# Optimization experiments

Hardware: AMD Instinct MI355X
Metric: run time of the kernel (lower is better)

## Reference

```python
import math
import jax, jax.numpy as jnp
import numpy as np

# Module hyperparameters (match init_kwargs)
EMBED = 512
H = 8            # n_heads
D = EMBED // H   # head_dim = 64
P = 32           # poly_dim
M = 4            # num_prf_features
R = 1            # num_quadrature_nodes
B = 1
T = 1024
EPS = 1e-6
C_CONST = 2.0 + EPS
# Gauss-Laguerre nodes/weights (R=1 -> node=1, weight=1), scaled by 1/C as in __init__
_nodes_np, _weights_np = np.polynomial.laguerre.laggauss(R)
QUAD_NODES = (_nodes_np / C_CONST).astype(np.float32)   # [R]


def setup_inputs() -> dict:
    key = jax.random.key(0)
    ks = jax.random.split(key, 6)
    x = jax.random.normal(ks[0], (B, T, EMBED), dtype=jnp.float32)
    qkv_w = jax.random.normal(ks[1], (3 * EMBED, EMBED), dtype=jnp.float32) * 0.02
    qkv_b = jnp.zeros((3 * EMBED,), dtype=jnp.float32)
    out_w = jax.random.normal(ks[2], (EMBED, EMBED), dtype=jnp.float32) * 0.02
    out_b = jnp.zeros((EMBED,), dtype=jnp.float32)
    omega = jax.random.normal(ks[3], (R, H, D, M), dtype=jnp.float32)  # PRF projection buffer
    poly_proj = jax.random.normal(ks[4], (H, D, P), dtype=jnp.float32) / math.sqrt(D)
    return {"x": x, "qkv_w": qkv_w, "qkv_b": qkv_b, "out_w": out_w,
            "out_b": out_b, "omega": omega, "poly_proj": poly_proj}


def _l2_normalize(z):
    # F.normalize(p=2, dim=-1), default eps=1e-12
    n = jnp.linalg.norm(z, axis=-1, keepdims=True)
    return z / jnp.maximum(n, 1e-12)


def _prf_features(x_norm, omega):
    # x_norm: [B,H,T,D], omega: [R,H,D,M] -> [R,B,H,T,M]
    proj = jnp.einsum('bhtd,rhdm->rbhtm', x_norm, omega)
    s = jnp.asarray(QUAD_NODES, x_norm.dtype).reshape(R, 1, 1, 1, 1)
    sqrt_2s = jnp.sqrt(2.0 * jnp.maximum(s, 0.0))
    exp_arg = jnp.clip(proj * sqrt_2s - s, -20.0, 20.0)
    return jnp.exp(exp_arg) / math.sqrt(M)


def _poly_features(x_norm, poly_proj):
    # squared random projection: [B,H,T,D] x [H,D,P] -> [B,H,T,P], nonneg
    p = jnp.einsum('bhtd,hdp->bhtp', x_norm, poly_proj)
    return p * p


def reference(x, qkv_w, qkv_b, out_w, out_b, omega, poly_proj):
    Bx, Tx, Cx = x.shape
    qkv = x @ qkv_w.T + qkv_b                       # [B,T,3C]
    q, k, v = jnp.split(qkv, 3, axis=-1)
    def to_heads(z):
        return z.reshape(Bx, Tx, H, D).transpose(0, 2, 1, 3)  # [B,H,T,D]
    q, k, v = to_heads(q), to_heads(k), to_heads(v)

    def full_features(z):
        zn = _l2_normalize(z)
        poly = _poly_features(zn, poly_proj)        # [B,H,T,P]
        prf = _prf_features(zn, omega)              # [R,B,H,T,M]
        return jnp.einsum('bhtp,rbhtm->rbhtpm', poly, prf)

    q_outer = full_features(q)                      # [R,B,H,T,P,M]
    k_outer = full_features(k)

    kv = jnp.einsum('rbhtpm,bhtd->rbhtpmd', k_outer, v)  # huge outer product
    kv_cumsum = jnp.cumsum(kv, axis=3)              # causal prefix sums along T
    k_cumsum = jnp.cumsum(k_outer, axis=3)

    context = jnp.einsum('rbhtpm,rbhtpmd->bhtd', q_outer, kv_cumsum)
    norm = jnp.einsum('rbhtpm,rbhtpm->bht', q_outer, k_cumsum)
    norm = jnp.maximum(norm, 1e-6)
    out = context / norm[..., None]                 # [B,H,T,D]

    out = out.transpose(0, 2, 1, 3).reshape(Bx, Tx, Cx)
    return out @ out_w.T + out_b
```

## Files before the change

kernel.cpp:

```cpp
#include <hip/hip_runtime.h>

#define T_LEN 1024
#define EMB   512
#define NH    8
#define HD    64
#define PDIM  32
#define MDIM  4
#define FDIM  128
#define TC    64
#define NC    16

typedef __attribute__((ext_vector_type(8))) short bf16x8;
typedef __attribute__((ext_vector_type(4))) float f32x4;

__device__ __forceinline__ unsigned short f2bf(float f) {
    unsigned u = __float_as_uint(f);
    unsigned r = u + 0x7fffu + ((u >> 16) & 1u);
    return (unsigned short)(r >> 16);
}
__device__ __forceinline__ float bf2f(unsigned short h) {
    return __uint_as_float(((unsigned)h) << 16);
}
__device__ __forceinline__ void split4(float4 v, ushort4& h4, ushort4& l4) {
    h4.x = f2bf(v.x); l4.x = f2bf(v.x - bf2f(h4.x));
    h4.y = f2bf(v.y); l4.y = f2bf(v.y - bf2f(h4.y));
    h4.z = f2bf(v.z); l4.z = f2bf(v.z - bf2f(h4.z));
    h4.w = f2bf(v.w); l4.w = f2bf(v.w - bf2f(h4.w));
}
__device__ __forceinline__ f32x4 mm3(bf16x8 ah, bf16x8 al, bf16x8 bh, bf16x8 bl, f32x4 acc) {
    acc = __builtin_amdgcn_mfma_f32_16x16x32_bf16(ah, bh, acc, 0, 0, 0);
    acc = __builtin_amdgcn_mfma_f32_16x16x32_bf16(ah, bl, acc, 0, 0, 0);
    acc = __builtin_amdgcn_mfma_f32_16x16x32_bf16(al, bh, acc, 0, 0, 0);
    return acc;
}
#define LD8(TILE, ROW, KB) (*reinterpret_cast<const bf16x8*>(&TILE[ROW][KB]))

__global__ __launch_bounds__(256) void k_cvt(
    const float* __restrict__ X, const float* __restrict__ Wq,
    const float* __restrict__ Wo,
    unsigned short* __restrict__ Xhi, unsigned short* __restrict__ Xlo,
    unsigned short* __restrict__ Whi, unsigned short* __restrict__ Wlo,
    unsigned short* __restrict__ Ohi, unsigned short* __restrict__ Olo)
{
    int i = (blockIdx.x * 256 + threadIdx.x) * 4;
    const float* src; unsigned short *dh, *dl; int off;
    if (i < 524288)       { src = X;  dh = Xhi; dl = Xlo; off = i; }
    else if (i < 1310720) { src = Wq; dh = Whi; dl = Wlo; off = i - 524288; }
    else                  { src = Wo; dh = Ohi; dl = Olo; off = i - 1310720; }
    float4 v = *reinterpret_cast<const float4*>(&src[off]);
    ushort4 h4, l4; split4(v, h4, l4);
    *reinterpret_cast<ushort4*>(&dh[off]) = h4;
    *reinterpret_cast<ushort4*>(&dl[off]) = l4;
}

__global__ __launch_bounds__(256) void k_qkv_mfma(
    const unsigned short* __restrict__ Xhi, const unsigned short* __restrict__ Xlo,
    const unsigned short* __restrict__ Whi, const unsigned short* __restrict__ Wlo,
    const float* __restrict__ bias,
    const float* __restrict__ poly_proj, const float* __restrict__ omega,
    unsigned short* __restrict__ Vhi, unsigned short* __restrict__ Vlo,
    unsigned short* __restrict__ qfhi, unsigned short* __restrict__ qflo,
    unsigned short* __restrict__ kfhi, unsigned short* __restrict__ kflo)
{
    const int j0 = blockIdx.x * 64;
    const int t0 = blockIdx.y * 64;
    __shared__ __align__(16) unsigned short Ahi[64][80], Alo[64][80],
                                            Bhi[64][80], Blo[64][80];
    __shared__ float poly_s[64][33];
    __shared__ float prf_s[64][5];
    __shared__ float nrm2[2][64];
    const int tid = threadIdx.x, lane = tid & 63, wid = tid >> 6;
    const int wrow = (wid >> 1) * 32, wcol = (wid & 1) * 32;
    const int lr = lane & 15, lg = lane >> 4;
    f32x4 acc[2][2];
    #pragma unroll
    for (int i = 0; i < 2; ++i)
        #pragma unroll
        for (int j = 0; j < 2; ++j) acc[i][j] = (f32x4){0.f, 0.f, 0.f, 0.f};

    for (int k0 = 0; k0 < 512; k0 += 64) {
        #pragma unroll
        for (int l = 0; l < 2; ++l) {
            int ch = tid + l * 256;
            int row = ch >> 3, sg = (ch & 7) * 8;
            size_t ao = (size_t)(t0 + row) * 512 + k0 + sg;
            size_t bo = (size_t)(j0 + row) * 512 + k0 + sg;
            *reinterpret_cast<int4*>(&Ahi[row][sg]) = *reinterpret_cast<const int4*>(&Xhi[ao]);
            *reinterpret_cast<int4*>(&Alo[row][sg]) = *reinterpret_cast<const int4*>(&Xlo[ao]);
            *reinterpret_cast<int4*>(&Bhi[row][sg]) = *reinterpret_cast<const int4*>(&Whi[bo]);
            *reinterpret_cast<int4*>(&Blo[row][sg]) = *reinterpret_cast<const int4*>(&Wlo[bo]);
        }
        __syncthreads();
        #pragma unroll
        for (int kh = 0; kh < 2; ++kh) {
            const int kb = kh * 32 + lg * 8;
            bf16x8 ah0 = LD8(Ahi, wrow + lr, kb),      ah1 = LD8(Ahi, wrow + 16 + lr, kb);
            bf16x8 al0 = LD8(Alo, wrow + lr, kb),      al1 = LD8(Alo, wrow + 16 + lr, kb);
            bf16x8 bh0 = LD8(Bhi, wcol + lr, kb),      bh1 = LD8(Bhi, wcol + 16 + lr, kb);
            bf16x8 bl0 = LD8(Blo, wcol + lr, kb),      bl1 = LD8(Blo, wcol + 16 + lr, kb);
            acc[0][0] = mm3(ah0, al0, bh0, bl0, acc[0][0]);
            acc[0][1] = mm3(ah0, al0, bh1, bl1, acc[0][1]);
            acc[1][0] = mm3(ah1, al1, bh0, bl0, acc[1][0]);
            acc[1][1] = mm3(ah1, al1, bh1, bl1, acc[1][1]);
        }
        __syncthreads();
    }
    const int which = j0 >> 9;
    const int h = (j0 & 511) >> 6;

    if (which == 2) {
        #pragma unroll
        for (int i = 0; i < 2; ++i)
            #pragma unroll
            for (int j = 0; j < 2; ++j)
                #pragma unroll
                for (int r = 0; r < 4; ++r) {
                    int row = wrow + i * 16 + lg * 4 + r;
                    int col = wcol + j * 16 + lr;
                    float val = acc[i][j][r] + bias[j0 + col];
                    unsigned short hv = f2bf(val);
                    size_t vi = (size_t)(h * T_LEN + t0 + row) * HD + col;
                    Vhi[vi] = hv; Vlo[vi] = f2bf(val - bf2f(hv));
                }
        return;
    }

    #pragma unroll
    for (int i = 0; i < 2; ++i) {
        #pragma unroll
        for (int r = 0; r < 4; ++r) {
            int row = wrow + i * 16 + lg * 4 + r;
            float ss = 0.f;
            #pragma unroll
            for (int j = 0; j < 2; ++j) {
                int col = wcol + j * 16 + lr;
                float zv = acc[i][j][r] + bias[j0 + col];
                ss = fmaf(zv, zv, ss);
                unsigned short hv = f2bf(zv);
                Ahi[row][col] = hv;
                Alo[row][col] = f2bf(zv - bf2f(hv));
            }
            ss += __shfl_xor(ss, 1, 64);
            ss += __shfl_xor(ss, 2, 64);
            ss += __shfl_xor(ss, 4, 64);
            ss += __shfl_xor(ss, 8, 64);
            if (lr == 0) nrm2[wid & 1][row] = ss;
        }
    }
    {
        const float* P = poly_proj + (size_t)h * 64 * 32;
        int d = tid >> 2, p8 = (tid & 3) * 8;
        #pragma unroll
        for (int e = 0; e < 8; ++e) {
            float pv = P[d * 32 + p8 + e];
            unsigned short hv = f2bf(pv);
            Bhi[p8 + e][d] = hv;
            Blo[p8 + e][d] = f2bf(pv - bf2f(hv));
        }
        if (tid < 64) {
            const float* Om = omega + (size_t)h * 64 * 4;
            float4 om = *reinterpret_cast<const float4*>(&Om[tid * 4]);
            float oa[4] = {om.x, om.y, om.z, om.w};
            #pragma unroll
            for (int m = 0; m < 4; ++m) {
                unsigned short hv = f2bf(oa[m]);
                Bhi[32 + m][tid] = hv;
                Blo[32 + m][tid] = f2bf(oa[m] - bf2f(hv));
            }
        }
        for (int rr = tid; rr < 12 * 64; rr += 256) {
            int row = 36 + (rr >> 6), dd = rr & 63;
            Bhi[row][dd] = 0; Blo[row][dd] = 0;
        }
    }
    __syncthreads();
    const int mrow = wid * 16;
    f32x4 g[3];
    g[0] = g[1] = g[2] = (f32x4){0.f, 0.f, 0.f, 0.f};
    #pragma unroll
    for (int kh = 0; kh < 2; ++kh) {
        const int kb = kh * 32 + lg * 8;
        bf16x8 ah = LD8(Ahi, mrow + lr, kb), al = LD8(Alo, mrow + lr, kb);
        #pragma unroll
        for (int j = 0; j < 3; ++j) {
            bf16x8 bh = LD8(Bhi, j * 16 + lr, kb), bl = LD8(Blo, j * 16 + lr, kb);
            g[j] = mm3(ah, al, bh, bl, g[j]);
        }
    }
    const float S_NODE = (float)(1.0 / 2.000001);
    const float SQRT2S = sqrtf(2.0f * S_NODE);
    #pragma unroll
    for (int r = 0; r < 4; ++r) {
        int row = mrow + lg * 4 + r;
        float rn = 1.0f / fmaxf(sqrtf(nrm2[0][row] + nrm2[1][row]), 1e-12f);
        #pragma unroll
        for (int j = 0; j < 3; ++j) {
            float gv = g[j][r] * rn;
            if (j < 2) poly_s[row][j * 16 + lr] = gv * gv;
            else if (lr < 4) {
                float arg = fminf(fmaxf(fmaf(gv, SQRT2S, -S_NODE), -20.0f), 20.0f);
                prf_s[row][lr] = expf(arg) * 0.5f;
            }
        }
    }
    {
        int row = mrow + (lane >> 2), fq = lane & 3;
        float pr[8], pf[4];
        #pragma unroll
        for (int e = 0; e < 8; ++e) pr[e] = poly_s[row][fq * 8 + e];
        #pragma unroll
        for (int m = 0; m < 4; ++m) pf[m] = prf_s[row][m];
        int4 hi4[4], lo4[4];
        unsigned short* hp = reinterpret_cast<unsigned short*>(hi4);
        unsigned short* lp = reinterpret_cast<unsigned short*>(lo4);
        #pragma unroll
        for (int e = 0; e < 8; ++e)
            #pragma unroll
            for (int m = 0; m < 4; ++m) {
                float val = pr[e] * pf[m];
                unsigned short hv = f2bf(val);
                hp[e * 4 + m] = hv;
                lp[e * 4 + m] = f2bf(val - bf2f(hv));
            }
        unsigned short* dhi = (which == 0) ? qfhi : kfhi;
        unsigned short* dlo = (which == 0) ? qflo : kflo;
        size_t base = (size_t)(h * T_LEN + t0 + row) * FDIM + fq * 32;
        #pragma unroll
        for (int s = 0; s < 4; ++s) {
            *reinterpret_cast<int4*>(&dhi[base + s * 8]) = hi4[s];
            *reinterpret_cast<int4*>(&dlo[base + s * 8]) = lo4[s];
        }
    }
}

__global__ __launch_bounds__(256) void k_out_mfma(
    const unsigned short* __restrict__ AThi, const unsigned short* __restrict__ ATlo,
    const unsigned short* __restrict__ Ohi, const unsigned short* __restrict__ Olo,
    const float* __restrict__ bias, float* __restrict__ Y)
{
    const int j0 = blockIdx.x * 64;
    const int t0 = blockIdx.y * 64;
    __shared__ __align__(16) unsigned short Ahi[64][80], Alo[64][80],
                                            Bhi[64][80], Blo[64][80];
    const int tid = threadIdx.x, lane = tid & 63, wid = tid >> 6;
    const int wrow = (wid >> 1) * 32, wcol = (wid & 1) * 32;
    const int lr = lane & 15, lg = lane >> 4;
    f32x4 acc[2][2];
    #pragma unroll
    for (int i = 0; i < 2; ++i)
        #pragma unroll
        for (int j = 0; j < 2; ++j) acc[i][j] = (f32x4){0.f, 0.f, 0.f, 0.f};

    for (int k0 = 0; k0 < 512; k0 += 64) {
        #pragma unroll
        for (int l = 0; l < 2; ++l) {
            int ch = tid + l * 256;
            int row = ch >> 3, sg = (ch & 7) * 8;
            size_t ao = (size_t)(t0 + row) * 512 + k0 + sg;
            size_t bo = (size_t)(j0 + row) * 512 + k0 + sg;
            *reinterpret_cast<int4*>(&Ahi[row][sg]) = *reinterpret_cast<const int4*>(&AThi[ao]);
            *reinterpret_cast<int4*>(&Alo[row][sg]) = *reinterpret_cast<const int4*>(&ATlo[ao]);
            *reinterpret_cast<int4*>(&Bhi[row][sg]) = *reinterpret_cast<const int4*>(&Ohi[bo]);
            *reinterpret_cast<int4*>(&Blo[row][sg]) = *reinterpret_cast<const int4*>(&Olo[bo]);
        }
        __syncthreads();
        #pragma unroll
        for (int kh = 0; kh < 2; ++kh) {
            const int kb = kh * 32 + lg * 8;
            bf16x8 ah0 = LD8(Ahi, wrow + lr, kb),      ah1 = LD8(Ahi, wrow + 16 + lr, kb);
            bf16x8 al0 = LD8(Alo, wrow + lr, kb),      al1 = LD8(Alo, wrow + 16 + lr, kb);
            bf16x8 bh0 = LD8(Bhi, wcol + lr, kb),      bh1 = LD8(Bhi, wcol + 16 + lr, kb);
            bf16x8 bl0 = LD8(Blo, wcol + lr, kb),      bl1 = LD8(Blo, wcol + 16 + lr, kb);
            acc[0][0] = mm3(ah0, al0, bh0, bl0, acc[0][0]);
            acc[0][1] = mm3(ah0, al0, bh1, bl1, acc[0][1]);
            acc[1][0] = mm3(ah1, al1, bh0, bl0, acc[1][0]);
            acc[1][1] = mm3(ah1, al1, bh1, bl1, acc[1][1]);
        }
        __syncthreads();
    }
    #pragma unroll
    for (int i = 0; i < 2; ++i)
        #pragma unroll
        for (int j = 0; j < 2; ++j)
            #pragma unroll
            for (int r = 0; r < 4; ++r) {
                int row = wrow + i * 16 + lg * 4 + r;
                int col = wcol + j * 16 + lr;
                Y[(size_t)(t0 + row) * EMB + j0 + col] = acc[i][j][r] + bias[j0 + col];
            }
}

__global__ __launch_bounds__(256) void k_chunk_kv(
    const unsigned short* __restrict__ kfhi, const unsigned short* __restrict__ kflo,
    const unsigned short* __restrict__ Vhi, const unsigned short* __restrict__ Vlo,
    float* __restrict__ Sch, float* __restrict__ zch)
{
    const int b = blockIdx.x;
    const int fh = b & 1, hc = b >> 1, h = hc >> 4, c = hc & 15;
    const int t0 = c * TC;
    const int tid = threadIdx.x, lane = tid & 63, wid = tid >> 6;
    const int wrow = (wid >> 1) * 32, wcol = (wid & 1) * 32;
    const int lr = lane & 15, lg = lane >> 4;
    __shared__ __align__(16) unsigned short Ahi[64][80], Alo[64][80],
                                            Bhi[64][80], Blo[64][80];
    #pragma unroll
    for (int l = 0; l < 2; ++l) {
        int ch = tid + l * 256;
        int t = ch >> 3, f8 = (ch & 7) * 8;
        int tb = t >> 3, tl = t & 7, m = f8 >> 3;
        size_t ko = (size_t)((h << 10) + t0 + t) * FDIM + fh * 64 + f8;
        int4 hv = *reinterpret_cast<const int4*>(&kfhi[ko]);
        int4 lv = *reinterpret_cast<const int4*>(&kflo[ko]);
        const unsigned short* hp = reinterpret_cast<const unsigned short*>(&hv);
        const unsigned short* lp = reinterpret_cast<const unsigned short*>(&lv);
        int col = ((tb ^ m) << 3) + tl;
        #pragma unroll
        for (int j = 0; j < 8; ++j) {
            Ahi[f8 + j][col] = hp[j];
            Alo[f8 + j][col] = lp[j];
        }
    }
    #pragma unroll
    for (int l = 0; l < 4; ++l) {
        int ch = tid + l * 256;
        int plane = ch >> 9, rem = ch & 511;
        int t = rem >> 3, d8 = (rem & 7) * 8;
        int tb = t >> 3, tl = t & 7;
        const unsigned short* src = plane ? Vlo : Vhi;
        int4 vv = *reinterpret_cast<const int4*>(&src[(size_t)((h << 10) + t0 + t) * HD + d8]);
        const unsigned short* vp = reinterpret_cast<const unsigned short*>(&vv);
        int col = ((tb ^ (d8 >> 3)) << 3) + tl;
        unsigned short (*dst)[80] = plane ? Blo : Bhi;
        #pragma unroll
        for (int j = 0; j < 8; ++j) dst[d8 + j][col] = vp[j];
    }
    __syncthreads();
    f32x4 acc[2][2];
    #pragma unroll
    for (int i = 0; i < 2; ++i)
        #pragma unroll
        for (int j = 0; j < 2; ++j) acc[i][j] = (f32x4){0.f, 0.f, 0.f, 0.f};
    #pragma unroll
    for (int kh = 0; kh < 2; ++kh) {
        const int kb = kh * 32 + lg * 8, cb = kb >> 3;
        const int d0 = wcol + lr, d1 = wcol + 16 + lr;
        const int c0 = ((cb ^ ((d0 >> 3) & 7)) << 3), c1 = ((cb ^ ((d1 >> 3) & 7)) << 3);
        bf16x8 bh0 = *reinterpret_cast<const bf16x8*>(&Bhi[d0][c0]);
        bf16x8 bl0 = *reinterpret_cast<const bf16x8*>(&Blo[d0][c0]);
        bf16x8 bh1 = *reinterpret_cast<const bf16x8*>(&Bhi[d1][c1]);
        bf16x8 bl1 = *reinterpret_cast<const bf16x8*>(&Blo[d1][c1]);
        #pragma unroll
        for (int fi = 0; fi < 2; ++fi) {
            int fr = wrow + fi * 16 + lr;
            int ca = ((cb ^ ((fr >> 3) & 7)) << 3);
            bf16x8 ah = *reinterpret_cast<const bf16x8*>(&Ahi[fr][ca]);
            bf16x8 al = *reinterpret_cast<const bf16x8*>(&Alo[fr][ca]);
            acc[fi][0] = mm3(ah, al, bh0, bl0, acc[fi][0]);
            acc[fi][1] = mm3(ah, al, bh1, bl1, acc[fi][1]);
        }
    }
    if (tid < 64) {
        float s = 0.f;
        const int g = (tid >> 3) & 7;
        #pragma unroll
        for (int cb2 = 0; cb2 < 8; ++cb2) {
            int base = ((cb2 ^ g) << 3);
            #pragma unroll
            for (int e = 0; e < 8; ++e)
                s += bf2f(Ahi[tid][base + e]) + bf2f(Alo[tid][base + e]);
        }
        zch[(h * NC + c) * FDIM + fh * 64 + tid] = s;
    }
    float* S = Sch + (size_t)(h * NC + c) * FDIM * HD;
    #pragma unroll
    for (int fi = 0; fi < 2; ++fi)
        #pragma unroll
        for (int dj = 0; dj < 2; ++dj)
            #pragma unroll
            for (int r = 0; r < 4; ++r) {
                int f = fh * 64 + wrow + fi * 16 + lg * 4 + r;
                int d = wcol + dj * 16 + lr;
                S[f * HD + d] = acc[fi][dj][r];
            }
}

__global__ __launch_bounds__(256) void k_prefix(
    const float* __restrict__ Sch, const float* __restrict__ zch,
    float* __restrict__ Spre, float* __restrict__ zpre)
{
    const int h = blockIdx.x >> 5;
    const int e = ((blockIdx.x & 31) << 8) + threadIdx.x;
    const size_t base = (size_t)h * NC * FDIM * HD + e;
    float vals[NC];
    #pragma unroll
    for (int c = 0; c < NC; ++c) vals[c] = Sch[base + (size_t)c * FDIM * HD];
    float run = 0.0f;
    #pragma unroll
    for (int c = 0; c < NC; ++c) {
        Spre[base + (size_t)c * FDIM * HD] = run;
        run += vals[c];
    }
    if ((blockIdx.x & 31) == 0 && threadIdx.x < FDIM) {
        const int zb = h * NC * FDIM + threadIdx.x;
        float zv[NC];
        #pragma unroll
        for (int c = 0; c < NC; ++c) zv[c] = zch[zb + c * FDIM];
        float zr = 0.0f;
        #pragma unroll
        for (int c = 0; c < NC; ++c) { zpre[zb + c * FDIM] = zr; zr += zv[c]; }
    }
}

__global__ __launch_bounds__(256) void k_attn_mfma(
    const unsigned short* __restrict__ qfhi, const unsigned short* __restrict__ qflo,
    const unsigned short* __restrict__ kfhi, const unsigned short* __restrict__ kflo,
    const float* __restrict__ Spre,
    const unsigned short* __restrict__ Vhi, const unsigned short* __restrict__ Vlo,
    const float* __restrict__ zpre,
    unsigned short* __restrict__ AThi, unsigned short* __restrict__ ATlo)
{
    const int b = blockIdx.x;
    const int h = b >> 5, c = (b >> 1) & 15, half = b & 1;
    const int tc0 = c * TC;
    const int tq0 = tc0 + half * 32;
    const int tid = threadIdx.x, lane = tid & 63, wid = tid >> 6;
    const int wrow = (wid >> 1) * 16, wcol = (wid & 1) * 32;
    const int lr = lane & 15, lg = lane >> 4;

    __shared__ __align__(16) unsigned short T0[32][80], T1[32][80];
    __shared__ __align__(16) unsigned short T2[64][80], T3[64][80];
    __shared__ __align__(16) unsigned short T4[64][80], T5[64][80];
    __shared__ unsigned short zhi[FDIM], zlo[FDIM];
    __shared__ float nrm_part[2][32], nrm[32];

    if (tid < FDIM) {
        float zv = zpre[(h * NC + c) * FDIM + tid];
        unsigned short zh = f2bf(zv);
        zhi[tid] = zh; zlo[tid] = f2bf(zv - bf2f(zh));
    }

    f32x4 accA[2], accC[2], accN;
    accA[0] = accA[1] = accC[0] = accC[1] = accN = (f32x4){0.f, 0.f, 0.f, 0.f};

    for (int f0 = 0; f0 < FDIM; f0 += 64) {
        {
            int row = tid >> 3, sg = (tid & 7) * 8;
            size_t qo = (size_t)(h * T_LEN + tq0 + row) * FDIM + f0 + sg;
            *reinterpret_cast<int4*>(&T0[row][sg]) = *reinterpret_cast<const int4*>(&qfhi[qo]);
            *reinterpret_cast<int4*>(&T1[row][sg]) = *reinterpret_cast<const int4*>(&qflo[qo]);
        }
        #pragma unroll
        for (int l = 0; l < 2; ++l) {
            int ch = tid + l * 256;
            int row = ch >> 3, sg = (ch & 7) * 8;
            size_t ko = (size_t)(h * T_LEN + tc0 + row) * FDIM + f0 + sg;
            *reinterpret_cast<int4*>(&T2[row][sg]) = *reinterpret_cast<const int4*>(&kfhi[ko]);
            *reinterpret_cast<int4*>(&T3[row][sg]) = *reinterpret_cast<const int4*>(&kflo[ko]);
        }
        #pragma unroll
        for (int l = 0; l < 4; ++l) {
            int ch = tid + l * 256;
            int f = ch >> 4, d4 = (ch & 15) * 4;
            int fb = f >> 3, fl = f & 7;
            float4 sv = *reinterpret_cast<const float4*>(
                &Spre[((size_t)((h * NC + c) * FDIM + f0 + f)) * HD + d4]);
            float arr[4] = {sv.x, sv.y, sv.z, sv.w};
            #pragma unroll
            for (int j = 0; j < 4; ++j) {
                int row = d4 + j;
                int col = ((fb ^ ((row >> 3) & 7)) << 3) + fl;
                unsigned short hv = f2bf(arr[j]);
                T4[row][col] = hv;
                T5[row][col] = f2bf(arr[j] - bf2f(hv));
            }
        }
        __syncthreads();
        #pragma unroll
        for (int kh = 0; kh < 2; ++kh) {
            const int kb = kh * 32 + lg * 8, cb = kb >> 3;
            bf16x8 qh = LD8(T0, wrow + lr, kb), ql = LD8(T1, wrow + lr, kb);
            bf16x8 kh0 = LD8(T2, wcol + lr, kb),      kh1 = LD8(T2, wcol + 16 + lr, kb);
            bf16x8 kl0 = LD8(T3, wcol + lr, kb),      kl1 = LD8(T3, wcol + 16 + lr, kb);
            const int d0 = wcol + lr, d1 = wcol + 16 + lr;
            const int c0 = ((cb ^ ((d0 >> 3) & 7)) << 3), c1 = ((cb ^ ((d1 >> 3) & 7)) << 3);
            bf16x8 sh0 = *reinterpret_cast<const bf16x8*>(&T4[d0][c0]);
            bf16x8 sl0 = *reinterpret_cast<const bf16x8*>(&T5[d0][c0]);
            bf16x8 sh1 = *reinterpret_cast<const bf16x8*>(&T4[d1][c1]);
            bf16x8 sl1 = *reinterpret_cast<const bf16x8*>(&T5[d1][c1]);
            accA[0] = mm3(qh, ql, kh0, kl0, accA[0]);
            accA[1] = mm3(qh, ql, kh1, kl1, accA[1]);
            accC[0] = mm3(qh, ql, sh0, sl0, accC[0]);
            accC[1] = mm3(qh, ql, sh1, sl1, accC[1]);
            bf16x8 zh8, zl8;
            #pragma unroll
            for (int j = 0; j < 8; ++j) {
                zh8[j] = (short)zhi[f0 + kb + j];
                zl8[j] = (short)zlo[f0 + kb + j];
            }
            accN = mm3(qh, ql, zh8, zl8, accN);
        }
        __syncthreads();
    }

    #pragma unroll
    for (int r = 0; r < 4; ++r) {
        int rowl = wrow + lg * 4 + r;
        int rowc = half * 32 + rowl;
        float rs = 0.f;
        #pragma unroll
        for (int j = 0; j < 2; ++j) {
            int col = wcol + j * 16 + lr;
            float vA = (col <= rowc) ? accA[j][r] : 0.f;
            rs += vA;
            unsigned short hv = f2bf(vA);
            T0[rowl][col] = hv;
            T1[rowl][col] = f2bf(vA - bf2f(hv));
        }
        #pragma unroll
        for (int off = 1; off < 16; off <<= 1) rs += __shfl_xor(rs, off, 64);
        if (lr == 0) {
            if ((wid & 1) == 0) nrm_part[0][rowl] = rs + accN[r];
            else                nrm_part[1][rowl] = rs;
        }
    }
    #pragma unroll
    for (int l = 0; l < 4; ++l) {
        int ch = tid + l * 256;
        int plane = ch >> 9, rem = ch & 511;
        int t = rem >> 3, d8 = (rem & 7) * 8;
        int tb = t >> 3, tl = t & 7;
        const unsigned short* src = plane ? Vlo : Vhi;
        int4 vv = *reinterpret_cast<const int4*>(&src[(size_t)(h * T_LEN + tc0 + t) * HD + d8]);
        const unsigned short* vp = reinterpret_cast<const unsigned short*>(&vv);
        int col = ((tb ^ (d8 >> 3)) << 3) + tl;
        unsigned short (*dst)[80] = plane ? T3 : T2;
        #pragma unroll
        for (int j = 0; j < 8; ++j) dst[d8 + j][col] = vp[j];
    }
    __syncthreads();
    if (tid < 32) nrm[tid] = fmaxf(nrm_part[0][tid] + nrm_part[1][tid], 1e-6f);

    #pragma unroll
    for (int kh = 0; kh < 2; ++kh) {
        const int kb = kh * 32 + lg * 8, cb = kb >> 3;
        bf16x8 ah = LD8(T0, wrow + lr, kb), al = LD8(T1, wrow + lr, kb);
        const int d0 = wcol + lr, d1 = wcol + 16 + lr;
        const int c0 = ((cb ^ ((d0 >> 3) & 7)) << 3), c1 = ((cb ^ ((d1 >> 3) & 7)) << 3);
        bf16x8 vh0 = *reinterpret_cast<const bf16x8*>(&T2[d0][c0]);
        bf16x8 vl0 = *reinterpret_cast<const bf16x8*>(&T3[d0][c0]);
        bf16x8 vh1 = *reinterpret_cast<const bf16x8*>(&T2[d1][c1]);
        bf16x8 vl1 = *reinterpret_cast<const bf16x8*>(&T3[d1][c1]);
        accC[0] = mm3(ah, al, vh0, vl0, accC[0]);
        accC[1] = mm3(ah, al, vh1, vl1, accC[1]);
    }
    __syncthreads();

    #pragma unroll
    for (int j = 0; j < 2; ++j)
        #pragma unroll
        for (int r = 0; r < 4; ++r) {
            int rowl = wrow + lg * 4 + r;
            int col = wcol + j * 16 + lr;
            float o = accC[j][r] / nrm[rowl];
            unsigned short hv = f2bf(o);
            size_t oi = (size_t)(tq0 + rowl) * EMB + h * HD + col;
            AThi[oi] = hv; ATlo[oi] = f2bf(o - bf2f(hv));
        }
}

extern "C" void kernel_launch(void* const* d_in, const int* in_sizes, int n_in,
                              void* d_out, int out_size, void* d_ws, size_t ws_size,
                              hipStream_t stream) {
    const float* x         = (const float*)d_in[0];
    const float* qkv_w     = (const float*)d_in[1];
    const float* qkv_b     = (const float*)d_in[2];
    const float* out_w     = (const float*)d_in[3];
    const float* out_b     = (const float*)d_in[4];
    const float* omega     = (const float*)d_in[5];
    const float* poly_proj = (const float*)d_in[6];
    float* out = (float*)d_out;

    unsigned short* Xhi  = (unsigned short*)d_ws;
    unsigned short* Xlo  = Xhi + 524288;
    unsigned short* Whi  = Xlo + 524288;
    unsigned short* Wlo  = Whi + 786432;
    unsigned short* Ohi  = Wlo + 786432;
    unsigned short* Olo  = Ohi + 262144;
    unsigned short* Vhi  = Olo + 262144;
    unsigned short* Vlo  = Vhi + 524288;
    unsigned short* qfhi = Vlo + 524288;
    unsigned short* qflo = qfhi + 1048576;
    unsigned short* kfhi = qflo + 1048576;
    unsigned short* kflo = kfhi + 1048576;
    float* Sch  = (float*)(kflo + 1048576);
    float* Spre = Sch + 1048576;
    float* zch  = Spre + 1048576;
    float* zpre = zch + 16384;
    unsigned short* AThi = Xhi;
    unsigned short* ATlo = Xlo;

    k_cvt<<<1536, 256, 0, stream>>>(x, qkv_w, out_w, Xhi, Xlo, Whi, Wlo, Ohi, Olo);
    k_qkv_mfma<<<dim3(24, 16), 256, 0, stream>>>(Xhi, Xlo, Whi, Wlo, qkv_b,
                                                 poly_proj, omega, Vhi, Vlo,
                                                 qfhi, qflo, kfhi, kflo);
    k_chunk_kv<<<256, 256, 0, stream>>>(kfhi, kflo, Vhi, Vlo, Sch, zch);
    k_prefix<<<256, 256, 0, stream>>>(Sch, zch, Spre, zpre);
    k_attn_mfma<<<NH * NC * 2, 256, 0, stream>>>(qfhi, qflo, kfhi, kflo, Spre,
                                                 Vhi, Vlo, zpre, AThi, ATlo);
    k_out_mfma<<<dim3(8, 16), 256, 0, stream>>>(AThi, ATlo, Ohi, Olo, out_b, out);
}
```

Measured before the change: 112.2 us.

## Store transposed prefix state and V in bf16 split form for vectorized attention loads

The chunk kernel now computes the chunk state transposed (d-major) and also writes a transposed bf16 hi/lo copy of V. The prefix kernel turns the running sums into bf16 hi/lo pairs with vectorized float2 loads and half as many blocks. The attention kernel can then load S and V tiles with int4 copies, where before it did scattered per-element transposes and float-to-bf16 conversions. This removes scalar LDS scatter and repeated conversion work, at the cost of extra global writes and reusing the Whi workspace region for the transposed V.

```diff
diff --git a/kernel.cpp b/kernel.cpp
--- a/kernel.cpp
+++ b/kernel.cpp
@@ -293,7 +293,8 @@
 __global__ __launch_bounds__(256) void k_chunk_kv(
     const unsigned short* __restrict__ kfhi, const unsigned short* __restrict__ kflo,
     const unsigned short* __restrict__ Vhi, const unsigned short* __restrict__ Vlo,
-    float* __restrict__ Sch, float* __restrict__ zch)
+    float* __restrict__ SchT, float* __restrict__ zch,
+    unsigned short* __restrict__ Vthi, unsigned short* __restrict__ Vtlo)
 {
     const int b = blockIdx.x;
     const int fh = b & 1, hc = b >> 1, h = hc >> 4, c = hc & 15;
@@ -301,8 +302,8 @@
     const int tid = threadIdx.x, lane = tid & 63, wid = tid >> 6;
     const int wrow = (wid >> 1) * 32, wcol = (wid & 1) * 32;
     const int lr = lane & 15, lg = lane >> 4;
-    __shared__ __align__(16) unsigned short Ahi[64][80], Alo[64][80],
-                                            Bhi[64][80], Blo[64][80];
+    __shared__ __align__(16) unsigned short Khi[64][80], Klo[64][80],
+                                            Ghi[64][80], Glo[64][80];
     #pragma unroll
     for (int l = 0; l < 2; ++l) {
         int ch = tid + l * 256;
@@ -316,8 +317,8 @@
         int col = ((tb ^ m) << 3) + tl;
         #pragma unroll
         for (int j = 0; j < 8; ++j) {
-            Ahi[f8 + j][col] = hp[j];
-            Alo[f8 + j][col] = lp[j];
+            Khi[f8 + j][col] = hp[j];
+            Klo[f8 + j][col] = lp[j];
         }
     }
     #pragma unroll
@@ -330,7 +331,7 @@
         int4 vv = *reinterpret_cast<const int4*>(&src[(size_t)((h << 10) + t0 + t) * HD + d8]);
         const unsigned short* vp = reinterpret_cast<const unsigned short*>(&vv);
         int col = ((tb ^ (d8 >> 3)) << 3) + tl;
-        unsigned short (*dst)[80] = plane ? Blo : Bhi;
+        unsigned short (*dst)[80] = plane ? Glo : Ghi;
         #pragma unroll
         for (int j = 0; j < 8; ++j) dst[d8 + j][col] = vp[j];
     }
@@ -343,20 +344,20 @@
     #pragma unroll
     for (int kh = 0; kh < 2; ++kh) {
         const int kb = kh * 32 + lg * 8, cb = kb >> 3;
-        const int d0 = wcol + lr, d1 = wcol + 16 + lr;
-        const int c0 = ((cb ^ ((d0 >> 3) & 7)) << 3), c1 = ((cb ^ ((d1 >> 3) & 7)) << 3);
-        bf16x8 bh0 = *reinterpret_cast<const bf16x8*>(&Bhi[d0][c0]);
-        bf16x8 bl0 = *reinterpret_cast<const bf16x8*>(&Blo[d0][c0]);
-        bf16x8 bh1 = *reinterpret_cast<const bf16x8*>(&Bhi[d1][c1]);
-        bf16x8 bl1 = *reinterpret_cast<const bf16x8*>(&Blo[d1][c1]);
-        #pragma unroll
-        for (int fi = 0; fi < 2; ++fi) {
-            int fr = wrow + fi * 16 + lr;
-            int ca = ((cb ^ ((fr >> 3) & 7)) << 3);
-            bf16x8 ah = *reinterpret_cast<const bf16x8*>(&Ahi[fr][ca]);
-            bf16x8 al = *reinterpret_cast<const bf16x8*>(&Alo[fr][ca]);
-            acc[fi][0] = mm3(ah, al, bh0, bl0, acc[fi][0]);
-            acc[fi][1] = mm3(ah, al, bh1, bl1, acc[fi][1]);
+        const int f0r = wcol + lr, f1r = wcol + 16 + lr;
+        const int c0 = ((cb ^ ((f0r >> 3) & 7)) << 3), c1 = ((cb ^ ((f1r >> 3) & 7)) << 3);
+        bf16x8 bh0 = *reinterpret_cast<const bf16x8*>(&Khi[f0r][c0]);
+        bf16x8 bl0 = *reinterpret_cast<const bf16x8*>(&Klo[f0r][c0]);
+        bf16x8 bh1 = *reinterpret_cast<const bf16x8*>(&Khi[f1r][c1]);
+        bf16x8 bl1 = *reinterpret_cast<const bf16x8*>(&Klo[f1r][c1]);
+        #pragma unroll
+        for (int di = 0; di < 2; ++di) {
+            int dr = wrow + di * 16 + lr;
+            int ca = ((cb ^ ((dr >> 3) & 7)) << 3);
+            bf16x8 ah = *reinterpret_cast<const bf16x8*>(&Ghi[dr][ca]);
+            bf16x8 al = *reinterpret_cast<const bf16x8*>(&Glo[dr][ca]);
+            acc[di][0] = mm3(ah, al, bh0, bl0, acc[di][0]);
+            acc[di][1] = mm3(ah, al, bh1, bl1, acc[di][1]);
         }
     }
     if (tid < 64) {
@@ -367,40 +368,59 @@
             int base = ((cb2 ^ g) << 3);
             #pragma unroll
             for (int e = 0; e < 8; ++e)
-                s += bf2f(Ahi[tid][base + e]) + bf2f(Alo[tid][base + e]);
+                s += bf2f(Khi[tid][base + e]) + bf2f(Klo[tid][base + e]);
         }
         zch[(h * NC + c) * FDIM + fh * 64 + tid] = s;
     }
-    float* S = Sch + (size_t)(h * NC + c) * FDIM * HD;
-    #pragma unroll
-    for (int fi = 0; fi < 2; ++fi)
-        #pragma unroll
-        for (int dj = 0; dj < 2; ++dj)
+    if (fh == 0) {
+        #pragma unroll
+        for (int l = 0; l < 4; ++l) {
+            int ch = tid + l * 256;
+            int plane = ch >> 9, rem = ch & 511;
+            int d = rem >> 3, m = rem & 7;
+            int g = (d >> 3) & 7;
+            const unsigned short (*src)[80] = plane ? Glo : Ghi;
+            unsigned short* dst = plane ? Vtlo : Vthi;
+            *reinterpret_cast<int4*>(&dst[(size_t)(h * HD + d) * T_LEN + t0 + ((m ^ g) << 3)]) =
+                *reinterpret_cast<const int4*>(&src[d][m << 3]);
+        }
+    }
+    float* S = SchT + (size_t)(h * NC + c) * FDIM * HD;
+    #pragma unroll
+    for (int di = 0; di < 2; ++di)
+        #pragma unroll
+        for (int fj = 0; fj < 2; ++fj)
             #pragma unroll
             for (int r = 0; r < 4; ++r) {
-                int f = fh * 64 + wrow + fi * 16 + lg * 4 + r;
-                int d = wcol + dj * 16 + lr;
-                S[f * HD + d] = acc[fi][dj][r];
+                int d = wrow + di * 16 + lg * 4 + r;
+                int f = fh * 64 + wcol + fj * 16 + lr;
+                S[d * FDIM + f] = acc[di][fj][r];
             }
 }
 
 __global__ __launch_bounds__(256) void k_prefix(
-    const float* __restrict__ Sch, const float* __restrict__ zch,
-    float* __restrict__ Spre, float* __restrict__ zpre)
+    const float* __restrict__ SchT, const float* __restrict__ zch,
+    unsigned short* __restrict__ SThi, unsigned short* __restrict__ STlo,
+    float* __restrict__ zpre)
 {
-    const int h = blockIdx.x >> 5;
-    const int e = ((blockIdx.x & 31) << 8) + threadIdx.x;
+    const int h = blockIdx.x >> 4;
+    const int e = ((blockIdx.x & 15) << 9) + threadIdx.x * 2;
     const size_t base = (size_t)h * NC * FDIM * HD + e;
-    float vals[NC];
-    #pragma unroll
-    for (int c = 0; c < NC; ++c) vals[c] = Sch[base + (size_t)c * FDIM * HD];
-    float run = 0.0f;
+    float2 vals[NC];
+    #pragma unroll
+    for (int c = 0; c < NC; ++c)
+        vals[c] = *reinterpret_cast<const float2*>(&SchT[base + (size_t)c * FDIM * HD]);
+    float r0 = 0.f, r1 = 0.f;
     #pragma unroll
     for (int c = 0; c < NC; ++c) {
-        Spre[base + (size_t)c * FDIM * HD] = run;
-        run += vals[c];
-    }
-    if ((blockIdx.x & 31) == 0 && threadIdx.x < FDIM) {
+        unsigned short h0 = f2bf(r0), h1 = f2bf(r1);
+        unsigned short l0 = f2bf(r0 - bf2f(h0)), l1 = f2bf(r1 - bf2f(h1));
+        size_t wi = base + (size_t)c * FDIM * HD;
+        *reinterpret_cast<unsigned*>(&SThi[wi]) = (unsigned)h0 | ((unsigned)h1 << 16);
+        *reinterpret_cast<unsigned*>(&STlo[wi]) = (unsigned)l0 | ((unsigned)l1 << 16);
+        r0 += vals[c].x; r1 += vals[c].y;
+    }
+    if ((blockIdx.x & 15) == 0 && threadIdx.x < FDIM) {
         const int zb = h * NC * FDIM + threadIdx.x;
         float zv[NC];
         #pragma unroll
@@ -414,8 +434,8 @@
 __global__ __launch_bounds__(256) void k_attn_mfma(
     const unsigned short* __restrict__ qfhi, const unsigned short* __restrict__ qflo,
     const unsigned short* __restrict__ kfhi, const unsigned short* __restrict__ kflo,
-    const float* __restrict__ Spre,
-    const unsigned short* __restrict__ Vhi, const unsigned short* __restrict__ Vlo,
+    const unsigned short* __restrict__ SThi, const unsigned short* __restrict__ STlo,
+    const unsigned short* __restrict__ Vthi, const unsigned short* __restrict__ Vtlo,
     const float* __restrict__ zpre,
     unsigned short* __restrict__ AThi, unsigned short* __restrict__ ATlo)
 {
@@ -458,35 +478,22 @@
             *reinterpret_cast<int4*>(&T3[row][sg]) = *reinterpret_cast<const int4*>(&kflo[ko]);
         }
         #pragma unroll
-        for (int l = 0; l < 4; ++l) {
+        for (int l = 0; l < 2; ++l) {
             int ch = tid + l * 256;
-            int f = ch >> 4, d4 = (ch & 15) * 4;
-            int fb = f >> 3, fl = f & 7;
-            float4 sv = *reinterpret_cast<const float4*>(
-                &Spre[((size_t)((h * NC + c) * FDIM + f0 + f)) * HD + d4]);
-            float arr[4] = {sv.x, sv.y, sv.z, sv.w};
-            #pragma unroll
-            for (int j = 0; j < 4; ++j) {
-                int row = d4 + j;
-                int col = ((fb ^ ((row >> 3) & 7)) << 3) + fl;
-                unsigned short hv = f2bf(arr[j]);
-                T4[row][col] = hv;
-                T5[row][col] = f2bf(arr[j] - bf2f(hv));
-            }
+            int row = ch >> 3, sg = (ch & 7) * 8;
+            size_t so = (size_t)(h * NC + c) * FDIM * HD + (size_t)row * FDIM + f0 + sg;
+            *reinterpret_cast<int4*>(&T4[row][sg]) = *reinterpret_cast<const int4*>(&SThi[so]);
+            *reinterpret_cast<int4*>(&T5[row][sg]) = *reinterpret_cast<const int4*>(&STlo[so]);
         }
         __syncthreads();
         #pragma unroll
         for (int kh = 0; kh < 2; ++kh) {
-            const int kb = kh * 32 + lg * 8, cb = kb >> 3;
+            const int kb = kh * 32 + lg * 8;
             bf16x8 qh = LD8(T0, wrow + lr, kb), ql = LD8(T1, wrow + lr, kb);
             bf16x8 kh0 = LD8(T2, wcol + lr, kb),      kh1 = LD8(T2, wcol + 16 + lr, kb);
             bf16x8 kl0 = LD8(T3, wcol + lr, kb),      kl1 = LD8(T3, wcol + 16 + lr, kb);
-            const int d0 = wcol + lr, d1 = wcol + 16 + lr;
-            const int c0 = ((cb ^ ((d0 >> 3) & 7)) << 3), c1 = ((cb ^ ((d1 >> 3) & 7)) << 3);
-            bf16x8 sh0 = *reinterpret_cast<const bf16x8*>(&T4[d0][c0]);
-            bf16x8 sl0 = *reinterpret_cast<const bf16x8*>(&T5[d0][c0]);
-            bf16x8 sh1 = *reinterpret_cast<const bf16x8*>(&T4[d1][c1]);
-            bf16x8 sl1 = *reinterpret_cast<const bf16x8*>(&T5[d1][c1]);
+            bf16x8 sh0 = LD8(T4, wcol + lr, kb),      sh1 = LD8(T4, wcol + 16 + lr, kb);
+            bf16x8 sl0 = LD8(T5, wcol + lr, kb),      sl1 = LD8(T5, wcol + 16 + lr, kb);
             accA[0] = mm3(qh, ql, kh0, kl0, accA[0]);
             accA[1] = mm3(qh, ql, kh1, kl1, accA[1]);
             accC[0] = mm3(qh, ql, sh0, sl0, accC[0]);
@@ -527,29 +534,21 @@
     for (int l = 0; l < 4; ++l) {
         int ch = tid + l * 256;
         int plane = ch >> 9, rem = ch & 511;
-        int t = rem >> 3, d8 = (rem & 7) * 8;
-        int tb = t >> 3, tl = t & 7;
-        const unsigned short* src = plane ? Vlo : Vhi;
-        int4 vv = *reinterpret_cast<const int4*>(&src[(size_t)(h * T_LEN + tc0 + t) * HD + d8]);
-        const unsigned short* vp = reinterpret_cast<const unsigned short*>(&vv);
-        int col = ((tb ^ (d8 >> 3)) << 3) + tl;
+        int row = rem >> 3, sg = (rem & 7) * 8;
+        size_t vo = (size_t)(h * HD + row) * T_LEN + tc0 + sg;
+        const unsigned short* src = plane ? Vtlo : Vthi;
         unsigned short (*dst)[80] = plane ? T3 : T2;
-        #pragma unroll
-        for (int j = 0; j < 8; ++j) dst[d8 + j][col] = vp[j];
+        *reinterpret_cast<int4*>(&dst[row][sg]) = *reinterpret_cast<const int4*>(&src[vo]);
     }
     __syncthreads();
     if (tid < 32) nrm[tid] = fmaxf(nrm_part[0][tid] + nrm_part[1][tid], 1e-6f);
 
     #pragma unroll
     for (int kh = 0; kh < 2; ++kh) {
-        const int kb = kh * 32 + lg * 8, cb = kb >> 3;
+        const int kb = kh * 32 + lg * 8;
         bf16x8 ah = LD8(T0, wrow + lr, kb), al = LD8(T1, wrow + lr, kb);
-        const int d0 = wcol + lr, d1 = wcol + 16 + lr;
-        const int c0 = ((cb ^ ((d0 >> 3) & 7)) << 3), c1 = ((cb ^ ((d1 >> 3) & 7)) << 3);
-        bf16x8 vh0 = *reinterpret_cast<const bf16x8*>(&T2[d0][c0]);
-        bf16x8 vl0 = *reinterpret_cast<const bf16x8*>(&T3[d0][c0]);
-        bf16x8 vh1 = *reinterpret_cast<const bf16x8*>(&T2[d1][c1]);
-        bf16x8 vl1 = *reinterpret_cast<const bf16x8*>(&T3[d1][c1]);
+        bf16x8 vh0 = LD8(T2, wcol + lr, kb),      vh1 = LD8(T2, wcol + 16 + lr, kb);
+        bf16x8 vl0 = LD8(T3, wcol + lr, kb),      vl1 = LD8(T3, wcol + 16 + lr, kb);
         accC[0] = mm3(ah, al, vh0, vl0, accC[0]);
         accC[1] = mm3(ah, al, vh1, vl1, accC[1]);
     }
@@ -592,20 +591,23 @@
     unsigned short* qflo = qfhi + 1048576;
     unsigned short* kfhi = qflo + 1048576;
     unsigned short* kflo = kfhi + 1048576;
-    float* Sch  = (float*)(kflo + 1048576);
-    float* Spre = Sch + 1048576;
-    float* zch  = Spre + 1048576;
+    float* SchT = (float*)(kflo + 1048576);
+    unsigned short* SThi = (unsigned short*)(SchT + 1048576);
+    unsigned short* STlo = SThi + 1048576;
+    float* zch  = (float*)(STlo + 1048576);
     float* zpre = zch + 16384;
     unsigned short* AThi = Xhi;
     unsigned short* ATlo = Xlo;
+    unsigned short* Vthi = Whi;
+    unsigned short* Vtlo = Whi + 524288;
 
     k_cvt<<<1536, 256, 0, stream>>>(x, qkv_w, out_w, Xhi, Xlo, Whi, Wlo, Ohi, Olo);
     k_qkv_mfma<<<dim3(24, 16), 256, 0, stream>>>(Xhi, Xlo, Whi, Wlo, qkv_b,
                                                  poly_proj, omega, Vhi, Vlo,
                                                  qfhi, qflo, kfhi, kflo);
-    k_chunk_kv<<<256, 256, 0, stream>>>(kfhi, kflo, Vhi, Vlo, Sch, zch);
-    k_prefix<<<256, 256, 0, stream>>>(Sch, zch, Spre, zpre);
-    k_attn_mfma<<<NH * NC * 2, 256, 0, stream>>>(qfhi, qflo, kfhi, kflo, Spre,
-                                                 Vhi, Vlo, zpre, AThi, ATlo);
+    k_chunk_kv<<<256, 256, 0, stream>>>(kfhi, kflo, Vhi, Vlo, SchT, zch, Vthi, Vtlo);
+    k_prefix<<<128, 256, 0, stream>>>(SchT, zch, SThi, STlo, zpre);
+    k_attn_mfma<<<NH * NC * 2, 256, 0, stream>>>(qfhi, qflo, kfhi, kflo, SThi, STlo,
+                                                 Vthi, Vtlo, zpre, AThi, ATlo);
     k_out_mfma<<<dim3(8, 16), 256, 0, stream>>>(AThi, ATlo, Ohi, Olo, out_b, out);
 }
```

Result: no change. 111.4 us (median of 2 runs) (-0.7%).
